# Kernel optimization log

Hardware: AMD Instinct MI355X
Metric: run time of the kernel (lower is better)

## Reference

```python
import jax, jax.numpy as jnp
import numpy as np

B, L, D, H = 2, 2048, 1024, 16
HD = D // H
KW = 4  # conv kernel width


def layernorm(x, g, b, eps=1e-5):
    m = jnp.mean(x, axis=-1, keepdims=True)
    v = jnp.var(x, axis=-1, keepdims=True)
    return (x - m) / jnp.sqrt(v + eps) * g + b


def causal_conv(x, w, b):
    # torch Conv1d(k=4, padding=3, groups=D) then truncate to L => causal depthwise conv
    # out[t] = sum_j w[:, j] * x[t - 3 + j] + b
    xp = jnp.pad(x, ((0, 0), (KW - 1, 0), (0, 0)))
    Lx = x.shape[1]
    out = b
    for j in range(KW):
        out = out + xp[:, j:j + Lx, :] * w[:, j]
    return out


def setup_inputs() -> dict:
    key = jax.random.key(0)
    ks = jax.random.split(key, 16)
    r = lambda i, shape, s=0.02: jax.random.normal(ks[i], shape, jnp.float32) * s
    return dict(
        x=r(0, (B, L, D), 1.0),
        Wqkv=r(1, (D, 3 * D)), Wout=r(2, (D, D)),
        Wgate=r(3, (D, D)), bgate=jnp.zeros((D,), jnp.float32),
        fn_g=jnp.ones((D,), jnp.float32), fn_b=jnp.zeros((D,), jnp.float32),
        dn_g=jnp.ones((D,), jnp.float32), dn_b=jnp.zeros((D,), jnp.float32),
        dWq=r(4, (D, D)), dWk=r(5, (D, D)), dWv=r(6, (D, D)), dWo=r(7, (D, D)),
        Wbeta=r(8, (D, H)), bbeta=jnp.zeros((H,), jnp.float32),
        cq_w=r(9, (D, KW), 0.1), cq_b=jnp.zeros((D,), jnp.float32),
        ck_w=r(10, (D, KW), 0.1), ck_b=jnp.zeros((D,), jnp.float32),
        ln_g=jnp.ones((D,), jnp.float32), ln_b=jnp.zeros((D,), jnp.float32),
    )


def _delta_scan(q, k, v, beta):
    # q,k,v: (B,L,H,HD) ; beta: (B,L,H)
    Bx = q.shape[0]
    S0 = jnp.zeros((Bx, H, HD, HD), q.dtype)
    z0 = jnp.zeros((Bx, H, HD), q.dtype)

    def step(carry, inp):
        S, z = carry
        q_t, k_t, v_t, b_t = inp  # (B,H,HD) x3, (B,H)
        y = jnp.einsum('bhij,bhj->bhi', S, q_t)
        denom = jnp.einsum('bhi,bhi->bh', z, q_t)[..., None] + 1e-6
        y = y / denom
        old = jnp.einsum('bhij,bhj->bhi', S, k_t)
        delta = v_t - old
        S = S + b_t[..., None, None] * jnp.einsum('bhi,bhj->bhij', delta, k_t)
        z = z + b_t[..., None] * k_t
        return (S, z), y

    xs = (jnp.moveaxis(q, 1, 0), jnp.moveaxis(k, 1, 0),
          jnp.moveaxis(v, 1, 0), jnp.moveaxis(beta, 1, 0))
    (S, z), ys = jax.lax.scan(step, (S0, z0), xs)
    return jnp.moveaxis(ys, 0, 1), S, z  # (B,L,H,HD)


def _forward(x, Wqkv, Wout, Wgate, bgate, fn_g, fn_b, dn_g, dn_b,
             dWq, dWk, dWv, dWo, Wbeta, bbeta, cq_w, cq_b, ck_w, ck_b, ln_g, ln_b):
    Bx, Lx, Dx = x.shape
    # ---- flash (full causal, L<=2048 branch) ----
    qkv = (x @ Wqkv).reshape(Bx, Lx, 3, H, HD)
    q = jnp.moveaxis(qkv[:, :, 0], 1, 2)  # (B,H,L,HD)
    k = jnp.moveaxis(qkv[:, :, 1], 1, 2)
    v = jnp.moveaxis(qkv[:, :, 2], 1, 2)
    scale = HD ** -0.5
    scores = jnp.einsum('bhqd,bhkd->bhqk', q, k) * scale
    causal = jnp.tril(jnp.ones((Lx, Lx), bool))
    scores = jnp.where(causal, scores, -jnp.inf)
    attn = jax.nn.softmax(scores, axis=-1)
    flash = jnp.einsum('bhqk,bhkd->bhqd', attn, v)
    flash = jnp.moveaxis(flash, 1, 2).reshape(Bx, Lx, Dx) @ Wout
    flash = layernorm(flash, fn_g, fn_b)
    # ---- delta branch ----
    dq = causal_conv(x @ dWq, cq_w, cq_b).reshape(Bx, Lx, H, HD)
    dk = causal_conv(x @ dWk, ck_w, ck_b).reshape(Bx, Lx, H, HD)
    dv = (x @ dWv).reshape(Bx, Lx, H, HD)
    dk = dk / jnp.maximum(jnp.linalg.norm(dk, axis=-1, keepdims=True), 1e-12)
    beta = jax.nn.sigmoid(x @ Wbeta + bbeta)  # (B,L,H)
    ys, S, z = _delta_scan(dq, dk, dv, beta)
    delta_out = layernorm(ys.reshape(Bx, Lx, Dx) @ dWo, ln_g, ln_b)  # DeltaAttention layer_norm
    delta_out = layernorm(delta_out, dn_g, dn_b)  # hybrid delta_norm
    # ---- gate ----
    gate = jax.nn.sigmoid(x @ Wgate + bgate)
    out = gate * flash + (1.0 - gate) * delta_out
    return out, S, z


def reference(x, Wqkv, Wout, Wgate, bgate, fn_g, fn_b, dn_g, dn_b,
              dWq, dWk, dWv, dWo, Wbeta, bbeta, cq_w, cq_b, ck_w, ck_b, ln_g, ln_b):
    return _forward(x, Wqkv, Wout, Wgate, bgate, fn_g, fn_b, dn_g, dn_b,
                    dWq, dWk, dWv, dWo, Wbeta, bbeta, cq_w, cq_b, ck_w, ck_b, ln_g, ln_b)
```

## Files before the change

kernel.cpp:

```cpp
#include <hip/hip_runtime.h>
#include <hip/hip_bf16.h>

constexpr int B_ = 2, L_ = 2048, D_ = 1024, H_ = 16;

using bf16x8 = __attribute__((ext_vector_type(8))) short;
using f32x4  = __attribute__((ext_vector_type(4))) float;

__device__ __forceinline__ short f2b(float f) {
  union { float f; unsigned int u; } v; v.f = f;
  unsigned int r = (v.u + 0x7FFFu + ((v.u >> 16) & 1u)) >> 16;
  return (short)r;
}
__device__ __forceinline__ float b2f(unsigned short h) {
  union { unsigned int u; float f; } v; v.u = ((unsigned int)h) << 16; return v.f;
}
__device__ __forceinline__ void split2(float x, float y, unsigned int& h, unsigned int& l) {
  unsigned short hx = (unsigned short)f2b(x), hy = (unsigned short)f2b(y);
  h = (unsigned int)hx | ((unsigned int)hy << 16);
  unsigned short lx = (unsigned short)f2b(x - b2f(hx)), ly = (unsigned short)f2b(y - b2f(hy));
  l = (unsigned int)lx | ((unsigned int)ly << 16);
}
__device__ __forceinline__ float dot4(float4 a, float4 b) {
  return a.x * b.x + a.y * b.y + a.z * b.z + a.w * b.w;
}

__global__ __launch_bounds__(256) void tcast(const float* __restrict__ W, short* __restrict__ Wt,
                                             int N, int K) {
  __shared__ float T[64][65];
  int n0 = blockIdx.x * 64, k0 = blockIdx.y * 64;
  int tid = threadIdx.x;
#pragma unroll
  for (int i = 0; i < 16; ++i) {
    int idx = i * 256 + tid;
    int r = idx >> 6, c = idx & 63;
    T[r][c] = W[(size_t)(k0 + r) * N + n0 + c];
  }
  __syncthreads();
#pragma unroll
  for (int i = 0; i < 16; ++i) {
    int idx = i * 256 + tid;
    int rr = idx >> 6, cc = idx & 63;
    Wt[(size_t)(n0 + rr) * K + k0 + cc] = f2b(T[cc][rr]);
  }
}

__global__ __launch_bounds__(256) void tcast2(const float* __restrict__ W1, const float* __restrict__ W2,
                                              short* __restrict__ Wt1, short* __restrict__ Wt2) {
  __shared__ float T[64][65];
  const float* W = blockIdx.z ? W2 : W1;
  short* Wt = blockIdx.z ? Wt2 : Wt1;
  int n0 = blockIdx.x * 64, k0 = blockIdx.y * 64;
  int tid = threadIdx.x;
#pragma unroll
  for (int i = 0; i < 16; ++i) {
    int idx = i * 256 + tid;
    int r = idx >> 6, c = idx & 63;
    T[r][c] = W[(size_t)(k0 + r) * 1024 + n0 + c];
  }
  __syncthreads();
#pragma unroll
  for (int i = 0; i < 16; ++i) {
    int idx = i * 256 + tid;
    int rr = idx >> 6, cc = idx & 63;
    Wt[(size_t)(n0 + rr) * 1024 + k0 + cc] = f2b(T[cc][rr]);
  }
}

__global__ __launch_bounds__(256) void tcast_split2(const float* __restrict__ W1, const float* __restrict__ W2,
                                                    short* __restrict__ Wh1, short* __restrict__ Wl1,
                                                    short* __restrict__ Wh2, short* __restrict__ Wl2) {
  __shared__ float T[64][65];
  const float* W = blockIdx.z ? W2 : W1;
  short* Wh = blockIdx.z ? Wh2 : Wh1;
  short* Wl = blockIdx.z ? Wl2 : Wl1;
  int n0 = blockIdx.x * 64, k0 = blockIdx.y * 64;
  int tid = threadIdx.x;
#pragma unroll
  for (int i = 0; i < 16; ++i) {
    int idx = i * 256 + tid;
    int r = idx >> 6, c = idx & 63;
    T[r][c] = W[(size_t)(k0 + r) * 1024 + n0 + c];
  }
  __syncthreads();
#pragma unroll
  for (int i = 0; i < 16; ++i) {
    int idx = i * 256 + tid;
    int rr = idx >> 6, cc = idx & 63;
    float w = T[cc][rr];
    short h = f2b(w);
    short l = f2b(w - b2f((unsigned short)h));
    size_t o = (size_t)(n0 + rr) * 1024 + k0 + cc;
    Wh[o] = h;
    Wl[o] = l;
  }
}

template <int BN, typename CT>
__device__ __forceinline__ void gemm_bt_body(const float* __restrict__ A, const short* __restrict__ Wt,
                                             CT* __restrict__ C, int N, int K, int bx, int by) {
  constexpr int MT = (BN == 128) ? 4 : 2;
  constexpr int NT = 4;
  __shared__ __align__(16) short As[128 * 32];
  __shared__ __align__(16) short Bs[BN * 32];
  int tid = threadIdx.x;
  int wave = tid >> 6, lane = tid & 63, quad = lane >> 4, l15 = lane & 15;
  int m0 = by * 128, n0 = bx * BN;
  int wm = (BN == 128) ? (wave >> 1) * 64 : wave * 32;
  int wn = (BN == 128) ? (wave & 1) * 64 : 0;
  f32x4 acc[MT][NT];
#pragma unroll
  for (int mt = 0; mt < MT; ++mt)
#pragma unroll
    for (int nt = 0; nt < NT; ++nt) acc[mt][nt] = (f32x4){0.f, 0.f, 0.f, 0.f};

  for (int k0 = 0; k0 < K; k0 += 32) {
    __syncthreads();
#pragma unroll
    for (int i = 0; i < 2; ++i) {
      int chunk = i * 256 + tid;
      int m = chunk >> 2, kc = (chunk & 3) * 8;
      const float* ap = A + (size_t)(m0 + m) * K + k0 + kc;
      float4 a0 = *(const float4*)ap;
      float4 a1 = *(const float4*)(ap + 4);
      __hip_bfloat162 c0 = __float22bfloat162_rn(make_float2(a0.x, a0.y));
      __hip_bfloat162 c1 = __float22bfloat162_rn(make_float2(a0.z, a0.w));
      __hip_bfloat162 c2 = __float22bfloat162_rn(make_float2(a1.x, a1.y));
      __hip_bfloat162 c3 = __float22bfloat162_rn(make_float2(a1.z, a1.w));
      uint4 u;
      u.x = *(unsigned int*)&c0; u.y = *(unsigned int*)&c1;
      u.z = *(unsigned int*)&c2; u.w = *(unsigned int*)&c3;
      *(uint4*)&As[m * 32 + kc] = u;
    }
#pragma unroll
    for (int i = 0; i < BN * 4 / 256; ++i) {
      int chunk = i * 256 + tid;
      int n = chunk >> 2, kc = (chunk & 3) * 8;
      uint4 w = *(const uint4*)(Wt + (size_t)(n0 + n) * K + k0 + kc);
      *(uint4*)&Bs[n * 32 + kc] = w;
    }
    __syncthreads();
    bf16x8 af[MT], bf[NT];
#pragma unroll
    for (int mt = 0; mt < MT; ++mt) af[mt] = *(bf16x8*)&As[(wm + mt * 16 + l15) * 32 + quad * 8];
#pragma unroll
    for (int nt = 0; nt < NT; ++nt) bf[nt] = *(bf16x8*)&Bs[(wn + nt * 16 + l15) * 32 + quad * 8];
#pragma unroll
    for (int mt = 0; mt < MT; ++mt)
#pragma unroll
      for (int nt = 0; nt < NT; ++nt)
        acc[mt][nt] = __builtin_amdgcn_mfma_f32_16x16x32_bf16(af[mt], bf[nt], acc[mt][nt], 0, 0, 0);
  }
#pragma unroll
  for (int mt = 0; mt < MT; ++mt)
#pragma unroll
    for (int nt = 0; nt < NT; ++nt)
#pragma unroll
      for (int r = 0; r < 4; ++r) {
        size_t idx = (size_t)(m0 + wm + mt * 16 + quad * 4 + r) * N + n0 + wn + nt * 16 + l15;
        if constexpr (sizeof(CT) == 2) C[idx] = f2b(acc[mt][nt][r]);
        else C[idx] = acc[mt][nt][r];
      }
}

template <int BN>
__global__ __launch_bounds__(256) void gemm_bt(const float* __restrict__ A, const short* __restrict__ Wt,
                                               float* __restrict__ C, int N, int K) {
  gemm_bt_body<BN, float>(A, Wt, C, N, K, blockIdx.x, blockIdx.y);
}

__global__ __launch_bounds__(256) void gemm_bt_h(const float* __restrict__ A, const short* __restrict__ Wt,
                                                 short* __restrict__ C, int N, int K) {
  gemm_bt_body<128, short>(A, Wt, C, N, K, blockIdx.x, blockIdx.y);
}

__global__ __launch_bounds__(256) void gemm_bt2(const float* __restrict__ A, const short* __restrict__ Wt1,
                                                const short* __restrict__ Wt2, float* __restrict__ C1,
                                                float* __restrict__ C2) {
  gemm_bt_body<64, float>(A, blockIdx.z ? Wt2 : Wt1, blockIdx.z ? C2 : C1, 1024, 1024,
                          blockIdx.x, blockIdx.y);
}

__global__ __launch_bounds__(256) void gemm_bt_split2(const float* __restrict__ A,
                                                      const short* __restrict__ Wh1, const short* __restrict__ Wl1,
                                                      const short* __restrict__ Wh2, const short* __restrict__ Wl2,
                                                      float* __restrict__ C1, float* __restrict__ C2) {
  constexpr int K = 1024, N = 1024;
  const short* Wh = blockIdx.z ? Wh2 : Wh1;
  const short* Wl = blockIdx.z ? Wl2 : Wl1;
  float* C = blockIdx.z ? C2 : C1;
  __shared__ __align__(16) short Ash[128 * 32];
  __shared__ __align__(16) short Asl[128 * 32];
  __shared__ __align__(16) short Bsh[64 * 32];
  __shared__ __align__(16) short Bsl[64 * 32];
  int tid = threadIdx.x;
  int wave = tid >> 6, lane = tid & 63, quad = lane >> 4, l15 = lane & 15;
  int m0 = blockIdx.y * 128, n0 = blockIdx.x * 64;
  int wm = wave * 32;
  f32x4 acc[2][4];
#pragma unroll
  for (int mt = 0; mt < 2; ++mt)
#pragma unroll
    for (int nt = 0; nt < 4; ++nt) acc[mt][nt] = (f32x4){0.f, 0.f, 0.f, 0.f};

  for (int k0 = 0; k0 < K; k0 += 32) {
    __syncthreads();
#pragma unroll
    for (int i = 0; i < 2; ++i) {
      int chunk = i * 256 + tid;
      int m = chunk >> 2, kc = (chunk & 3) * 8;
      const float* ap = A + (size_t)(m0 + m) * K + k0 + kc;
      float4 a0 = *(const float4*)ap;
      float4 a1 = *(const float4*)(ap + 4);
      uint4 uh, ul;
      split2(a0.x, a0.y, uh.x, ul.x);
      split2(a0.z, a0.w, uh.y, ul.y);
      split2(a1.x, a1.y, uh.z, ul.z);
      split2(a1.z, a1.w, uh.w, ul.w);
      *(uint4*)&Ash[m * 32 + kc] = uh;
      *(uint4*)&Asl[m * 32 + kc] = ul;
    }
    {
      int n = tid >> 2, kc = (tid & 3) * 8;
      size_t off = (size_t)(n0 + n) * K + k0 + kc;
      *(uint4*)&Bsh[n * 32 + kc] = *(const uint4*)(Wh + off);
      *(uint4*)&Bsl[n * 32 + kc] = *(const uint4*)(Wl + off);
    }
    __syncthreads();
    bf16x8 ah[2], al[2], bh[4], bl[4];
#pragma unroll
    for (int mt = 0; mt < 2; ++mt) {
      ah[mt] = *(bf16x8*)&Ash[(wm + mt * 16 + l15) * 32 + quad * 8];
      al[mt] = *(bf16x8*)&Asl[(wm + mt * 16 + l15) * 32 + quad * 8];
    }
#pragma unroll
    for (int nt = 0; nt < 4; ++nt) {
      bh[nt] = *(bf16x8*)&Bsh[(nt * 16 + l15) * 32 + quad * 8];
      bl[nt] = *(bf16x8*)&Bsl[(nt * 16 + l15) * 32 + quad * 8];
    }
#pragma unroll
    for (int mt = 0; mt < 2; ++mt)
#pragma unroll
      for (int nt = 0; nt < 4; ++nt) {
        f32x4 a = acc[mt][nt];
        a = __builtin_amdgcn_mfma_f32_16x16x32_bf16(al[mt], bh[nt], a, 0, 0, 0);
        a = __builtin_amdgcn_mfma_f32_16x16x32_bf16(ah[mt], bl[nt], a, 0, 0, 0);
        a = __builtin_amdgcn_mfma_f32_16x16x32_bf16(ah[mt], bh[nt], a, 0, 0, 0);
        acc[mt][nt] = a;
      }
  }
#pragma unroll
  for (int mt = 0; mt < 2; ++mt)
#pragma unroll
    for (int nt = 0; nt < 4; ++nt)
#pragma unroll
      for (int r = 0; r < 4; ++r) {
        size_t idx = (size_t)(m0 + wm + mt * 16 + quad * 4 + r) * N + n0 + nt * 16 + l15;
        C[idx] = acc[mt][nt][r];
      }
}

__global__ __launch_bounds__(256) void attn_mfma(const short* __restrict__ qkv, float* __restrict__ outp) {
  __shared__ __align__(16) short Kl[64 * 64];
  __shared__ __align__(16) short Vt[64 * 64];
  __shared__ __align__(16) short Pl[64 * 64];
  int qb = 31 - blockIdx.x, h = blockIdx.y, b = blockIdx.z;
  int tid = threadIdx.x;
  int wave = tid >> 6, lane = tid & 63;
  int quad = lane >> 4, l15 = lane & 15;
  int qrow = qb * 64 + wave * 16 + l15;
  bf16x8 qf[2];
  {
    const short* qbase = qkv + (size_t)(b * L_ + qrow) * 3072 + h * 64;
#pragma unroll
    for (int s = 0; s < 2; ++s) qf[s] = *(const bf16x8*)(qbase + s * 32 + quad * 8);
  }
  f32x4 Of[4];
  float mrow[4], lrow[4], alpha[4];
#pragma unroll
  for (int dt = 0; dt < 4; ++dt) Of[dt] = (f32x4){0.f, 0.f, 0.f, 0.f};
#pragma unroll
  for (int r = 0; r < 4; ++r) { mrow[r] = -1e30f; lrow[r] = 0.f; }

  for (int kt = 0; kt <= qb; ++kt) {
    __syncthreads();
#pragma unroll
    for (int it = 0; it < 2; ++it) {
      int e8 = tid + it * 256;
      int key = e8 >> 3, g = e8 & 7;
      const short* src = qkv + ((size_t)((b * L_ + kt * 64 + key) * 3) + 1) * 1024 + h * 64 + g * 8;
      *(bf16x8*)&Kl[key * 64 + ((g ^ (key & 7)) << 3)] = *(const bf16x8*)src;
    }
    {
      int key4 = tid >> 4;
      int d4 = tid & 15;
      const short* vsrc = qkv + ((size_t)((b * L_ + kt * 64 + key4 * 4) * 3) + 2) * 1024 + h * 64 + d4 * 4;
      short4 v0 = *(const short4*)vsrc;
      short4 v1 = *(const short4*)(vsrc + 3072);
      short4 v2 = *(const short4*)(vsrc + 6144);
      short4 v3 = *(const short4*)(vsrc + 9216);
      short vr0[4] = {v0.x, v0.y, v0.z, v0.w};
      short vr1[4] = {v1.x, v1.y, v1.z, v1.w};
      short vr2[4] = {v2.x, v2.y, v2.z, v2.w};
      short vr3[4] = {v3.x, v3.y, v3.z, v3.w};
      int kg = key4 >> 1, k7b = (key4 & 1) * 4;
#pragma unroll
      for (int jj = 0; jj < 4; ++jj) {
        int d = d4 * 4 + jj;
        short4 sv;
        sv.x = vr0[jj]; sv.y = vr1[jj]; sv.z = vr2[jj]; sv.w = vr3[jj];
        *(short4*)&Vt[d * 64 + ((kg ^ (d & 7)) << 3) + k7b] = sv;
      }
    }
    __syncthreads();
    f32x4 sc[4];
#pragma unroll
    for (int nt = 0; nt < 4; ++nt) sc[nt] = (f32x4){0.f, 0.f, 0.f, 0.f};
#pragma unroll
    for (int s = 0; s < 2; ++s) {
#pragma unroll
      for (int nt = 0; nt < 4; ++nt) {
        int key = nt * 16 + l15;
        bf16x8 kf = *(bf16x8*)&Kl[key * 64 + (((4 * s + quad) ^ (key & 7)) << 3)];
        sc[nt] = __builtin_amdgcn_mfma_f32_16x16x32_bf16(qf[s], kf, sc[nt], 0, 0, 0);
      }
    }
    bool diag = (kt == qb);
#pragma unroll
    for (int r = 0; r < 4; ++r) {
      float sv[4];
#pragma unroll
      for (int nt = 0; nt < 4; ++nt) {
        float v = sc[nt][r] * 0.125f;
        if (diag && (nt * 16 + l15 > wave * 16 + quad * 4 + r)) v = -1e30f;
        sv[nt] = v;
      }
      float mx = fmaxf(fmaxf(sv[0], sv[1]), fmaxf(sv[2], sv[3]));
      mx = fmaxf(mx, __shfl_xor(mx, 1));
      mx = fmaxf(mx, __shfl_xor(mx, 2));
      mx = fmaxf(mx, __shfl_xor(mx, 4));
      mx = fmaxf(mx, __shfl_xor(mx, 8));
      float mnew = fmaxf(mrow[r], mx);
      float al = __expf(mrow[r] - mnew);
      mrow[r] = mnew;
      alpha[r] = al;
      int prow = wave * 16 + quad * 4 + r;
      int r7 = prow & 7;
      float ps = 0.f;
#pragma unroll
      for (int nt = 0; nt < 4; ++nt) {
        float p = __expf(sv[nt] - mnew);
        ps += p;
        Pl[prow * 64 + ((((nt << 1) + (l15 >> 3)) ^ r7) << 3) + (l15 & 7)] = f2b(p);
      }
      ps += __shfl_xor(ps, 1);
      ps += __shfl_xor(ps, 2);
      ps += __shfl_xor(ps, 4);
      ps += __shfl_xor(ps, 8);
      lrow[r] = lrow[r] * al + ps;
    }
#pragma unroll
    for (int dt = 0; dt < 4; ++dt)
#pragma unroll
      for (int r = 0; r < 4; ++r) Of[dt][r] *= alpha[r];
#pragma unroll
    for (int s = 0; s < 2; ++s) {
      bf16x8 pf = *(bf16x8*)&Pl[(wave * 16 + l15) * 64 + (((4 * s + quad) ^ (l15 & 7)) << 3)];
#pragma unroll
      for (int dt = 0; dt < 4; ++dt) {
        int d = dt * 16 + l15;
        bf16x8 vf = *(bf16x8*)&Vt[d * 64 + (((4 * s + quad) ^ (d & 7)) << 3)];
        Of[dt] = __builtin_amdgcn_mfma_f32_16x16x32_bf16(pf, vf, Of[dt], 0, 0, 0);
      }
    }
  }
#pragma unroll
  for (int r = 0; r < 4; ++r) alpha[r] = 1.f / lrow[r];
  int orow = qb * 64 + wave * 16 + quad * 4;
#pragma unroll
  for (int dt = 0; dt < 4; ++dt)
#pragma unroll
    for (int r = 0; r < 4; ++r)
      outp[(size_t)(b * L_ + orow + r) * 1024 + h * 64 + dt * 16 + l15] = Of[dt][r] * alpha[r];
}

__global__ __launch_bounds__(256) void ln_kernel(float* __restrict__ X, const float* __restrict__ g,
                                                 const float* __restrict__ bb) {
  int row = blockIdx.x, tid = threadIdx.x;
  float* xr = X + (size_t)row * D_;
  float v[4], s = 0.f, ss = 0.f;
#pragma unroll
  for (int i = 0; i < 4; ++i) { v[i] = xr[tid + i * 256]; s += v[i]; ss += v[i] * v[i]; }
#pragma unroll
  for (int off = 32; off; off >>= 1) { s += __shfl_xor(s, off); ss += __shfl_xor(ss, off); }
  __shared__ float rs[4], rss[4];
  if ((tid & 63) == 0) { rs[tid >> 6] = s; rss[tid >> 6] = ss; }
  __syncthreads();
  float S = rs[0] + rs[1] + rs[2] + rs[3];
  float SS = rss[0] + rss[1] + rss[2] + rss[3];
  float mean = S * (1.f / 1024.f);
  float var = SS * (1.f / 1024.f) - mean * mean;
  float inv = rsqrtf(var + 1e-5f);
#pragma unroll
  for (int i = 0; i < 4; ++i) {
    int c = tid + i * 256;
    xr[c] = (v[i] - mean) * inv * g[c] + bb[c];
  }
}

__global__ __launch_bounds__(256) void ln2mix_kernel(const float* __restrict__ X,
                                                     const float* __restrict__ g1, const float* __restrict__ b1,
                                                     const float* __restrict__ g2, const float* __restrict__ b2,
                                                     const float* __restrict__ gpre, const float* __restrict__ bgate,
                                                     const float* __restrict__ fo, float* __restrict__ outp) {
  int row = blockIdx.x, tid = threadIdx.x;
  const float* xr = X + (size_t)row * D_;
  __shared__ float rs[4], rss[4];
  float v[4], s = 0.f, ss = 0.f;
#pragma unroll
  for (int i = 0; i < 4; ++i) { v[i] = xr[tid + i * 256]; s += v[i]; ss += v[i] * v[i]; }
#pragma unroll
  for (int off = 32; off; off >>= 1) { s += __shfl_xor(s, off); ss += __shfl_xor(ss, off); }
  if ((tid & 63) == 0) { rs[tid >> 6] = s; rss[tid >> 6] = ss; }
  __syncthreads();
  float S = rs[0] + rs[1] + rs[2] + rs[3];
  float SS = rss[0] + rss[1] + rss[2] + rss[3];
  float mean = S * (1.f / 1024.f);
  float var = SS * (1.f / 1024.f) - mean * mean;
  float inv = rsqrtf(var + 1e-5f);
  s = 0.f; ss = 0.f;
#pragma unroll
  for (int i = 0; i < 4; ++i) {
    int c = tid + i * 256;
    v[i] = (v[i] - mean) * inv * g1[c] + b1[c];
    s += v[i]; ss += v[i] * v[i];
  }
#pragma unroll
  for (int off = 32; off; off >>= 1) { s += __shfl_xor(s, off); ss += __shfl_xor(ss, off); }
  __syncthreads();
  if ((tid & 63) == 0) { rs[tid >> 6] = s; rss[tid >> 6] = ss; }
  __syncthreads();
  S = rs[0] + rs[1] + rs[2] + rs[3];
  SS = rss[0] + rss[1] + rss[2] + rss[3];
  mean = S * (1.f / 1024.f);
  var = SS * (1.f / 1024.f) - mean * mean;
  inv = rsqrtf(var + 1e-5f);
#pragma unroll
  for (int i = 0; i < 4; ++i) {
    int c = tid + i * 256;
    size_t idx = (size_t)row * D_ + c;
    float w = (v[i] - mean) * inv * g2[c] + b2[c];
    float gg = 1.f / (1.f + __expf(-(gpre[idx] + bgate[c])));
    outp[idx] = gg * fo[idx] + (1.f - gg) * w;
  }
}

__global__ __launch_bounds__(256) void convnorm_kernel(const float* __restrict__ qin, const float* __restrict__ kin,
                                                       const float* __restrict__ qw, const float* __restrict__ qb,
                                                       const float* __restrict__ kw, const float* __restrict__ kb,
                                                       float* __restrict__ qout, float* __restrict__ kout) {
  int path = blockIdx.y;
  int row = blockIdx.x * 4 + (threadIdx.x >> 6);
  int lane = threadIdx.x & 63;
  int bl = row >> 4, h = row & 15;
  int t = bl & (L_ - 1);
  int d = h * 64 + lane;
  size_t idx = (size_t)bl * D_ + d;
  const float* xin = path ? kin : qin;
  const float* w = path ? kw : qw;
  const float* bias = path ? kb : qb;
  float acc = bias[d];
#pragma unroll
  for (int j = 0; j < 4; ++j) {
    int tt = t - 3 + j;
    if (tt >= 0) acc += w[d * 4 + j] * xin[idx + (size_t)(j - 3) * D_];
  }
  if (path) {
    float n2 = acc * acc;
#pragma unroll
    for (int off = 32; off; off >>= 1) n2 += __shfl_xor(n2, off);
    acc = acc / fmaxf(sqrtf(n2), 1e-12f);
    kout[idx] = acc;
  } else {
    qout[idx] = acc;
  }
}

__global__ __launch_bounds__(256) void beta_kernel(const float* __restrict__ xf, const float* __restrict__ Wb,
                                                   const float* __restrict__ bb, float* __restrict__ beta) {
  int row = blockIdx.x, tid = threadIdx.x;
  int h = tid & 15, seg = tid >> 4;
  const float* xr = xf + (size_t)row * D_ + seg * 64;
  const float* wp = Wb + (seg * 64) * H_ + h;
  float p = 0.f;
  for (int k = 0; k < 64; ++k) p += xr[k] * wp[k * H_];
  __shared__ float red[16][17];
  red[seg][h] = p;
  __syncthreads();
  if (tid < 16) {
    float s = bb[tid];
#pragma unroll
    for (int s2 = 0; s2 < 16; ++s2) s += red[s2][tid];
    beta[(size_t)row * H_ + tid] = 1.f / (1.f + __expf(-s));
  }
}

__global__ __launch_bounds__(256) void prep_kernel(const float* __restrict__ dq, const float* __restrict__ dk,
                                                   const float* __restrict__ beta,
                                                   float* __restrict__ Minv_g, float* __restrict__ Bq_g) {
  __shared__ __align__(16) float Kl[32 * 68];
  __shared__ __align__(16) float Ql[32 * 68];
  __shared__ __align__(16) float Ml[32 * 36];
  __shared__ __align__(16) float Xl[32 * 36];
  __shared__ __align__(16) float bl[32];
  int c = blockIdx.x, bh = blockIdx.y;
  int b = bh >> 4, h = bh & 15;
  int t0 = c * 32;
  int tid = threadIdx.x;
#pragma unroll
  for (int rep = 0; rep < 2; ++rep) {
    int id = tid * 2 + rep;
    int r = id >> 4, j4 = id & 15;
    size_t gi = (size_t)(b * L_ + t0 + r) * 1024 + h * 64 + j4 * 4;
    *(float4*)&Kl[r * 68 + j4 * 4] = *(const float4*)&dk[gi];
    *(float4*)&Ql[r * 68 + j4 * 4] = *(const float4*)&dq[gi];
  }
  if (tid < 32) bl[tid] = beta[(size_t)(b * L_ + t0 + tid) * 16 + h];
  __syncthreads();
  int t = tid >> 3, s0 = (tid & 7) * 4;
  float accA[4] = {0.f, 0.f, 0.f, 0.f}, accB[4] = {0.f, 0.f, 0.f, 0.f};
#pragma unroll
  for (int k4 = 0; k4 < 16; ++k4) {
    float4 kt = *(float4*)&Kl[t * 68 + k4 * 4];
    float4 qt = *(float4*)&Ql[t * 68 + k4 * 4];
#pragma unroll
    for (int j = 0; j < 4; ++j) {
      float4 ks = *(float4*)&Kl[(s0 + j) * 68 + k4 * 4];
      accA[j] += dot4(kt, ks);
      accB[j] += dot4(qt, ks);
    }
  }
  float4 bq;
  float* bqp = (float*)&bq;
#pragma unroll
  for (int j = 0; j < 4; ++j) {
    int s = s0 + j;
    Ml[t * 36 + s] = (s < t) ? bl[t] * accA[j] : ((s == t) ? 1.f : 0.f);
    bqp[j] = (s < t) ? accB[j] : 0.f;
  }
  size_t obase = ((size_t)(bh * 64 + c) * 32 + t) * 32 + s0;
  *(float4*)&Bq_g[obase] = bq;
  __syncthreads();
  if (tid < 32) {
    int col = tid;
    float xr[32];
#pragma unroll
    for (int tt = 0; tt < 32; ++tt) {
      float x = (tt == col) ? 1.f : 0.f;
#pragma unroll
      for (int s = 0; s < tt; ++s) x -= Ml[tt * 36 + s] * xr[s];
      xr[tt] = x;
      Xl[tt * 36 + col] = x;
    }
  }
  __syncthreads();
  float4 mv = make_float4(Xl[t * 36 + s0], Xl[t * 36 + s0 + 1], Xl[t * 36 + s0 + 2], Xl[t * 36 + s0 + 3]);
  *(float4*)&Minv_g[obase] = mv;
}

__global__ __launch_bounds__(256) void delta_kernel(const float* __restrict__ dq, const float* __restrict__ dk,
                                                    const float* __restrict__ dv, const float* __restrict__ beta,
                                                    const float* __restrict__ Minv_g, const float* __restrict__ Bq_g,
                                                    float* __restrict__ ys, float* __restrict__ outS,
                                                    float* __restrict__ outZ) {
  __shared__ __align__(16) float Kl[2][32 * 68];
  __shared__ __align__(16) float Ql[2][32 * 68];
  __shared__ __align__(16) float Vl[2][32 * 9];
  __shared__ __align__(16) float Mil[2][32 * 36];
  __shared__ __align__(16) float Bql[2][32 * 36];
  __shared__ __align__(16) float bl[2][32];
  __shared__ __align__(16) float S0l[8 * 68];
  __shared__ __align__(16) float Y0l[32 * 9];
  __shared__ __align__(16) float RtmpTl[8 * 36];
  __shared__ __align__(16) float RTl[8 * 36];
  __shared__ __align__(16) float z0l[68];
  __shared__ __align__(16) float qzl[32];
  __shared__ __align__(16) float denl[32];
  int bh = blockIdx.x & 31, grp = blockIdx.x >> 5;
  int b = bh >> 4, h = bh & 15;
  int i0 = grp * 8;
  int tid = threadIdx.x;
  int r = tid >> 3, j8 = (tid & 7) * 8, s4 = tid & 7;
  size_t kqbase = (size_t)(b * L_) * 1024 + h * 64;

  for (int e = tid; e < 8 * 68; e += 256) S0l[e] = 0.f;
  if (tid < 68) z0l[tid] = 0.f;

  float4 kA, kB, qA, qB, mr, br;
  float vr, blr = 0.f;
  {
    const float* kp = dk + kqbase + (size_t)r * 1024 + j8;
    kA = ((const float4*)kp)[0]; kB = ((const float4*)kp)[1];
    const float* qp = dq + kqbase + (size_t)r * 1024 + j8;
    qA = ((const float4*)qp)[0]; qB = ((const float4*)qp)[1];
    size_t gb = ((size_t)(bh * 64) * 32 + r) * 32 + s4 * 4;
    mr = *(const float4*)&Minv_g[gb];
    br = *(const float4*)&Bq_g[gb];
    vr = dv[(size_t)(b * L_ + r) * 1024 + h * 64 + i0 + s4];
    if (tid < 32) blr = beta[(size_t)(b * L_ + tid) * 16 + h];
  }
  *(float4*)&Kl[0][r * 68 + j8] = kA; *(float4*)&Kl[0][r * 68 + j8 + 4] = kB;
  *(float4*)&Ql[0][r * 68 + j8] = qA; *(float4*)&Ql[0][r * 68 + j8 + 4] = qB;
  *(float4*)&Mil[0][r * 36 + s4 * 4] = mr;
  *(float4*)&Bql[0][r * 36 + s4 * 4] = br;
  Vl[0][r * 9 + s4] = vr;
  if (tid < 32) bl[0][tid] = blr;
  __syncthreads();

  for (int c = 0; c < 64; ++c) {
    int cur = c & 1, nxt = cur ^ 1;
    int cn = (c + 1 < 64) ? c + 1 : 63;
    int t0n = cn * 32;
    {
      const float* kp = dk + kqbase + (size_t)(t0n + r) * 1024 + j8;
      kA = ((const float4*)kp)[0]; kB = ((const float4*)kp)[1];
      const float* qp = dq + kqbase + (size_t)(t0n + r) * 1024 + j8;
      qA = ((const float4*)qp)[0]; qB = ((const float4*)qp)[1];
      size_t gb = ((size_t)(bh * 64 + cn) * 32 + r) * 32 + s4 * 4;
      mr = *(const float4*)&Minv_g[gb];
      br = *(const float4*)&Bq_g[gb];
      vr = dv[(size_t)(b * L_ + t0n + r) * 1024 + h * 64 + i0 + s4];
      if (tid < 32) blr = beta[(size_t)(b * L_ + t0n + tid) * 16 + h];
    }
    int t0 = c * 32;
    {
      int rr = tid >> 3;
      int iq = (tid >> 1) & 3;
      int jh = tid & 1;
      float aK0 = 0.f, aK1 = 0.f, aY0 = 0.f, aY1 = 0.f;
#pragma unroll
      for (int jj = 0; jj < 8; ++jj) {
        int j4 = jh * 8 + jj;
        float4 k = *(float4*)&Kl[cur][rr * 68 + j4 * 4];
        float4 q = *(float4*)&Ql[cur][rr * 68 + j4 * 4];
        float4 sA = *(float4*)&S0l[iq * 68 + j4 * 4];
        float4 sB = *(float4*)&S0l[(iq + 4) * 68 + j4 * 4];
        aK0 += dot4(k, sA); aK1 += dot4(k, sB);
        aY0 += dot4(q, sA); aY1 += dot4(q, sB);
      }
      aK0 += __shfl_xor(aK0, 1); aK1 += __shfl_xor(aK1, 1);
      aY0 += __shfl_xor(aY0, 1); aY1 += __shfl_xor(aY1, 1);
      if (jh == 0) {
        float be = bl[cur][rr];
        RtmpTl[iq * 36 + rr] = be * (Vl[cur][rr * 9 + iq] - aK0);
        RtmpTl[(iq + 4) * 36 + rr] = be * (Vl[cur][rr * 9 + iq + 4] - aK1);
        Y0l[rr * 9 + iq] = aY0;
        Y0l[rr * 9 + iq + 4] = aY1;
      }
      if (tid < 32) {
        float a = 0.f;
#pragma unroll
        for (int j4 = 0; j4 < 16; ++j4) {
          float4 q = *(float4*)&Ql[cur][tid * 68 + j4 * 4];
          float4 z = *(float4*)&z0l[j4 * 4];
          a += dot4(q, z);
        }
        qzl[tid] = a;
      }
    }
    __syncthreads();
    {
      int t = tid >> 3, i = tid & 7;
      float acc = 0.f;
#pragma unroll
      for (int s4i = 0; s4i < 8; ++s4i) {
        float4 m = *(float4*)&Mil[cur][t * 36 + s4i * 4];
        float4 rt = *(float4*)&RtmpTl[i * 36 + s4i * 4];
        acc += dot4(m, rt);
      }
      RTl[i * 36 + t] = acc;
      if (tid < 32) {
        float a = qzl[tid];
#pragma unroll
        for (int s4i = 0; s4i < 8; ++s4i) {
          float4 bq = *(float4*)&Bql[cur][tid * 36 + s4i * 4];
          float4 be = *(float4*)&bl[cur][s4i * 4];
          a += dot4(bq, be);
        }
        denl[tid] = a + 1e-6f;
      }
    }
    __syncthreads();
    {
      int t = tid >> 3, i = tid & 7;
      float acc = 0.f;
#pragma unroll
      for (int s4i = 0; s4i < 8; ++s4i) {
        float4 bq = *(float4*)&Bql[cur][t * 36 + s4i * 4];
        float4 rt = *(float4*)&RTl[i * 36 + s4i * 4];
        acc += dot4(bq, rt);
      }
      float y = (Y0l[t * 9 + i] + acc) / denl[t];
      ys[(size_t)(b * L_ + t0 + t) * 1024 + h * 64 + i0 + i] = y;
    }
    {
      int i = tid >> 5;
      int j2 = (tid & 31) * 2;
      float a0 = S0l[i * 68 + j2];
      float a1 = S0l[i * 68 + j2 + 1];
#pragma unroll
      for (int s4i = 0; s4i < 8; ++s4i) {
        float4 rt = *(float4*)&RTl[i * 36 + s4i * 4];
        float2 k0 = *(float2*)&Kl[cur][(s4i * 4 + 0) * 68 + j2];
        float2 k1 = *(float2*)&Kl[cur][(s4i * 4 + 1) * 68 + j2];
        float2 k2 = *(float2*)&Kl[cur][(s4i * 4 + 2) * 68 + j2];
        float2 k3 = *(float2*)&Kl[cur][(s4i * 4 + 3) * 68 + j2];
        a0 += rt.x * k0.x + rt.y * k1.x + rt.z * k2.x + rt.w * k3.x;
        a1 += rt.x * k0.y + rt.y * k1.y + rt.z * k2.y + rt.w * k3.y;
      }
      S0l[i * 68 + j2] = a0;
      S0l[i * 68 + j2 + 1] = a1;
    }
    if (tid < 64) {
      float a = z0l[tid];
#pragma unroll
      for (int s = 0; s < 32; ++s) a += bl[cur][s] * Kl[cur][s * 68 + tid];
      z0l[tid] = a;
    }
    *(float4*)&Kl[nxt][r * 68 + j8] = kA; *(float4*)&Kl[nxt][r * 68 + j8 + 4] = kB;
    *(float4*)&Ql[nxt][r * 68 + j8] = qA; *(float4*)&Ql[nxt][r * 68 + j8 + 4] = qB;
    *(float4*)&Mil[nxt][r * 36 + s4 * 4] = mr;
    *(float4*)&Bql[nxt][r * 36 + s4 * 4] = br;
    Vl[nxt][r * 9 + s4] = vr;
    if (tid < 32) bl[nxt][tid] = blr;
    __syncthreads();
  }
  {
    int i = tid >> 5, j2 = (tid & 31) * 2;
    *(float2*)&outS[((size_t)(bh * 64) + i0 + i) * 64 + j2] = *(float2*)&S0l[i * 68 + j2];
  }
  if (grp == 0 && tid < 64) outZ[bh * 64 + tid] = z0l[tid];
}

extern "C" void kernel_launch(void* const* d_in, const int* in_sizes, int n_in,
                              void* d_out, int out_size, void* d_ws, size_t ws_size,
                              hipStream_t stream) {
  const float* x     = (const float*)d_in[0];
  const float* Wqkv  = (const float*)d_in[1];
  const float* Wout  = (const float*)d_in[2];
  const float* Wgate = (const float*)d_in[3];
  const float* bgate = (const float*)d_in[4];
  const float* fn_g  = (const float*)d_in[5];
  const float* fn_b  = (const float*)d_in[6];
  const float* dn_g  = (const float*)d_in[7];
  const float* dn_b  = (const float*)d_in[8];
  const float* dWq   = (const float*)d_in[9];
  const float* dWk   = (const float*)d_in[10];
  const float* dWv   = (const float*)d_in[11];
  const float* dWo   = (const float*)d_in[12];
  const float* Wbeta = (const float*)d_in[13];
  const float* bbeta = (const float*)d_in[14];
  const float* cq_w  = (const float*)d_in[15];
  const float* cq_b  = (const float*)d_in[16];
  const float* ck_w  = (const float*)d_in[17];
  const float* ck_b  = (const float*)d_in[18];
  const float* ln_g  = (const float*)d_in[19];
  const float* ln_b  = (const float*)d_in[20];

  float* ws = (float*)d_ws;
  short* qkvh   = (short*)ws;
  float* dv     = ws;
  float* dqc    = ws + 4194304;
  float* dkc    = ws + 8388608;
  float* attnO  = ws + 12582912;
  short* wtg    = (short*)(ws + 12582912);
  short* Wvt    = (short*)(ws + 14680064);
  float* Minv_g = ws + 12582912;
  float* Bq_g   = ws + 14680064;
  float* do1    = ws + 12582912;
  float* fo     = ws + 16777216;
  float* dqp    = ws + 20971520;
  float* gpre   = ws + 20971520;
  float* dkp    = ws + 25165824;
  float* ysb    = ws + 25165824;
  float* betab  = ws + 29360128;

  short* Wqkvt = (short*)(ws + 20971520);
  short* Woutt = (short*)(ws + 29426688);
  short* Wot   = (short*)(ws + 4194304);

  short* Wqh = (short*)(ws + 8388608);
  short* Wql = (short*)(ws + 8912896);
  short* Wkh = (short*)(ws + 9437184);
  short* Wkl = (short*)(ws + 9961472);

  float* out  = (float*)d_out;
  float* outS = out + 4194304;
  float* outZ = out + 4325376;

  tcast<<<dim3(48, 16), 256, 0, stream>>>(Wqkv, Wqkvt, 3072, 1024);
  gemm_bt_h<<<dim3(24, 32), 256, 0, stream>>>(x, Wqkvt, qkvh, 3072, 1024);
  attn_mfma<<<dim3(32, H_, B_), 256, 0, stream>>>(qkvh, attnO);
  tcast<<<dim3(16, 16), 256, 0, stream>>>(Wout, Woutt, 1024, 1024);
  gemm_bt<64><<<dim3(16, 32), 256, 0, stream>>>(attnO, Woutt, fo, 1024, 1024);
  ln_kernel<<<4096, 256, 0, stream>>>(fo, fn_g, fn_b);
  tcast_split2<<<dim3(16, 16, 2), 256, 0, stream>>>(dWq, dWk, Wqh, Wql, Wkh, Wkl);
  gemm_bt_split2<<<dim3(16, 32, 2), 256, 0, stream>>>(x, Wqh, Wql, Wkh, Wkl, dqp, dkp);
  convnorm_kernel<<<dim3(16384, 2), 256, 0, stream>>>(dqp, dkp, cq_w, cq_b, ck_w, ck_b, dqc, dkc);
  beta_kernel<<<4096, 256, 0, stream>>>(x, Wbeta, bbeta, betab);
  tcast2<<<dim3(16, 16, 2), 256, 0, stream>>>(dWv, Wgate, Wvt, wtg);
  gemm_bt2<<<dim3(16, 32, 2), 256, 0, stream>>>(x, Wvt, wtg, dv, gpre);
  prep_kernel<<<dim3(64, 32), 256, 0, stream>>>(dqc, dkc, betab, Minv_g, Bq_g);
  delta_kernel<<<256, 256, 0, stream>>>(dqc, dkc, dv, betab, Minv_g, Bq_g, ysb, outS, outZ);
  tcast<<<dim3(16, 16), 256, 0, stream>>>(dWo, Wot, 1024, 1024);
  gemm_bt<64><<<dim3(16, 32), 256, 0, stream>>>(ysb, Wot, do1, 1024, 1024);
  ln2mix_kernel<<<4096, 256, 0, stream>>>(do1, ln_g, ln_b, dn_g, dn_b, gpre, bgate, fo, out);
}
```

Measured before the change: 806.3 us.

## Split delta scan over more blocks with 4 state rows each, single-buffer LDS

The delta-rule chunked scan kernel now assigns 4 rows of the state matrix per block instead of 8, doubling the grid from 256 to 512 blocks to fill more compute units on the sequential chunk loop. Shared-memory double buffering is dropped in favor of single buffers plus an extra barrier before staging the next chunk, shrinking LDS use. Each block still redundantly loads the full K, Q, Minv and Bq tiles and recomputes the z/denominator, so global traffic for those grows, and half the threads sit idle in several phases.

Result: faster. 778.2 us (-3.5%).

```diff
diff --git a/kernel.cpp b/kernel.cpp
--- a/kernel.cpp
+++ b/kernel.cpp
@@ -572,31 +572,31 @@
                                                     const float* __restrict__ Minv_g, const float* __restrict__ Bq_g,
                                                     float* __restrict__ ys, float* __restrict__ outS,
                                                     float* __restrict__ outZ) {
-  __shared__ __align__(16) float Kl[2][32 * 68];
-  __shared__ __align__(16) float Ql[2][32 * 68];
-  __shared__ __align__(16) float Vl[2][32 * 9];
-  __shared__ __align__(16) float Mil[2][32 * 36];
-  __shared__ __align__(16) float Bql[2][32 * 36];
-  __shared__ __align__(16) float bl[2][32];
-  __shared__ __align__(16) float S0l[8 * 68];
-  __shared__ __align__(16) float Y0l[32 * 9];
-  __shared__ __align__(16) float RtmpTl[8 * 36];
-  __shared__ __align__(16) float RTl[8 * 36];
+  __shared__ __align__(16) float Kl[32 * 68];
+  __shared__ __align__(16) float Ql[32 * 68];
+  __shared__ __align__(16) float Vl[32 * 5];
+  __shared__ __align__(16) float Mil[32 * 36];
+  __shared__ __align__(16) float Bql[32 * 36];
+  __shared__ __align__(16) float bl[32];
+  __shared__ __align__(16) float S0l[4 * 68];
+  __shared__ __align__(16) float Y0l[32 * 5];
+  __shared__ __align__(16) float RtmpTl[4 * 36];
+  __shared__ __align__(16) float RTl[4 * 36];
   __shared__ __align__(16) float z0l[68];
   __shared__ __align__(16) float qzl[32];
   __shared__ __align__(16) float denl[32];
   int bh = blockIdx.x & 31, grp = blockIdx.x >> 5;
   int b = bh >> 4, h = bh & 15;
-  int i0 = grp * 8;
+  int i0 = grp * 4;
   int tid = threadIdx.x;
   int r = tid >> 3, j8 = (tid & 7) * 8, s4 = tid & 7;
   size_t kqbase = (size_t)(b * L_) * 1024 + h * 64;
 
-  for (int e = tid; e < 8 * 68; e += 256) S0l[e] = 0.f;
+  for (int e = tid; e < 4 * 68; e += 256) S0l[e] = 0.f;
   if (tid < 68) z0l[tid] = 0.f;
 
   float4 kA, kB, qA, qB, mr, br;
-  float vr, blr = 0.f;
+  float vr = 0.f, blr = 0.f;
   {
     const float* kp = dk + kqbase + (size_t)r * 1024 + j8;
     kA = ((const float4*)kp)[0]; kB = ((const float4*)kp)[1];
@@ -605,19 +605,18 @@
     size_t gb = ((size_t)(bh * 64) * 32 + r) * 32 + s4 * 4;
     mr = *(const float4*)&Minv_g[gb];
     br = *(const float4*)&Bq_g[gb];
-    vr = dv[(size_t)(b * L_ + r) * 1024 + h * 64 + i0 + s4];
+    if (tid < 128) vr = dv[(size_t)(b * L_ + (tid >> 2)) * 1024 + h * 64 + i0 + (tid & 3)];
     if (tid < 32) blr = beta[(size_t)(b * L_ + tid) * 16 + h];
   }
-  *(float4*)&Kl[0][r * 68 + j8] = kA; *(float4*)&Kl[0][r * 68 + j8 + 4] = kB;
-  *(float4*)&Ql[0][r * 68 + j8] = qA; *(float4*)&Ql[0][r * 68 + j8 + 4] = qB;
-  *(float4*)&Mil[0][r * 36 + s4 * 4] = mr;
-  *(float4*)&Bql[0][r * 36 + s4 * 4] = br;
-  Vl[0][r * 9 + s4] = vr;
-  if (tid < 32) bl[0][tid] = blr;
+  *(float4*)&Kl[r * 68 + j8] = kA; *(float4*)&Kl[r * 68 + j8 + 4] = kB;
+  *(float4*)&Ql[r * 68 + j8] = qA; *(float4*)&Ql[r * 68 + j8 + 4] = qB;
+  *(float4*)&Mil[r * 36 + s4 * 4] = mr;
+  *(float4*)&Bql[r * 36 + s4 * 4] = br;
+  if (tid < 128) Vl[(tid >> 2) * 5 + (tid & 3)] = vr;
+  if (tid < 32) bl[tid] = blr;
   __syncthreads();
 
   for (int c = 0; c < 64; ++c) {
-    int cur = c & 1, nxt = cur ^ 1;
     int cn = (c + 1 < 64) ? c + 1 : 63;
     int t0n = cn * 32;
     {
@@ -628,39 +627,36 @@
       size_t gb = ((size_t)(bh * 64 + cn) * 32 + r) * 32 + s4 * 4;
       mr = *(const float4*)&Minv_g[gb];
       br = *(const float4*)&Bq_g[gb];
-      vr = dv[(size_t)(b * L_ + t0n + r) * 1024 + h * 64 + i0 + s4];
+      if (tid < 128) vr = dv[(size_t)(b * L_ + t0n + (tid >> 2)) * 1024 + h * 64 + i0 + (tid & 3)];
       if (tid < 32) blr = beta[(size_t)(b * L_ + t0n + tid) * 16 + h];
     }
     int t0 = c * 32;
     {
-      int rr = tid >> 3;
-      int iq = (tid >> 1) & 3;
       int jh = tid & 1;
-      float aK0 = 0.f, aK1 = 0.f, aY0 = 0.f, aY1 = 0.f;
+      int i = (tid >> 1) & 3;
+      int t = tid >> 3;
+      float aK = 0.f, aY = 0.f;
 #pragma unroll
       for (int jj = 0; jj < 8; ++jj) {
         int j4 = jh * 8 + jj;
-        float4 k = *(float4*)&Kl[cur][rr * 68 + j4 * 4];
-        float4 q = *(float4*)&Ql[cur][rr * 68 + j4 * 4];
-        float4 sA = *(float4*)&S0l[iq * 68 + j4 * 4];
-        float4 sB = *(float4*)&S0l[(iq + 4) * 68 + j4 * 4];
-        aK0 += dot4(k, sA); aK1 += dot4(k, sB);
-        aY0 += dot4(q, sA); aY1 += dot4(q, sB);
-      }
-      aK0 += __shfl_xor(aK0, 1); aK1 += __shfl_xor(aK1, 1);
-      aY0 += __shfl_xor(aY0, 1); aY1 += __shfl_xor(aY1, 1);
+        float4 k = *(float4*)&Kl[t * 68 + j4 * 4];
+        float4 q = *(float4*)&Ql[t * 68 + j4 * 4];
+        float4 s = *(float4*)&S0l[i * 68 + j4 * 4];
+        aK += dot4(k, s);
+        aY += dot4(q, s);
+      }
+      aK += __shfl_xor(aK, 1);
+      aY += __shfl_xor(aY, 1);
       if (jh == 0) {
-        float be = bl[cur][rr];
-        RtmpTl[iq * 36 + rr] = be * (Vl[cur][rr * 9 + iq] - aK0);
-        RtmpTl[(iq + 4) * 36 + rr] = be * (Vl[cur][rr * 9 + iq + 4] - aK1);
-        Y0l[rr * 9 + iq] = aY0;
-        Y0l[rr * 9 + iq + 4] = aY1;
+        float be = bl[t];
+        RtmpTl[i * 36 + t] = be * (Vl[t * 5 + i] - aK);
+        Y0l[t * 5 + i] = aY;
       }
       if (tid < 32) {
         float a = 0.f;
 #pragma unroll
         for (int j4 = 0; j4 < 16; ++j4) {
-          float4 q = *(float4*)&Ql[cur][tid * 68 + j4 * 4];
+          float4 q = *(float4*)&Ql[tid * 68 + j4 * 4];
           float4 z = *(float4*)&z0l[j4 * 4];
           a += dot4(q, z);
         }
@@ -669,74 +665,73 @@
     }
     __syncthreads();
     {
-      int t = tid >> 3, i = tid & 7;
-      float acc = 0.f;
-#pragma unroll
-      for (int s4i = 0; s4i < 8; ++s4i) {
-        float4 m = *(float4*)&Mil[cur][t * 36 + s4i * 4];
-        float4 rt = *(float4*)&RtmpTl[i * 36 + s4i * 4];
-        acc += dot4(m, rt);
-      }
-      RTl[i * 36 + t] = acc;
-      if (tid < 32) {
-        float a = qzl[tid];
+      if (tid < 128) {
+        int t = tid >> 2, i = tid & 3;
+        float acc = 0.f;
 #pragma unroll
         for (int s4i = 0; s4i < 8; ++s4i) {
-          float4 bq = *(float4*)&Bql[cur][tid * 36 + s4i * 4];
-          float4 be = *(float4*)&bl[cur][s4i * 4];
+          float4 m = *(float4*)&Mil[t * 36 + s4i * 4];
+          float4 rt = *(float4*)&RtmpTl[i * 36 + s4i * 4];
+          acc += dot4(m, rt);
+        }
+        RTl[i * 36 + t] = acc;
+      } else if (tid < 160) {
+        int t = tid - 128;
+        float a = qzl[t];
+#pragma unroll
+        for (int s4i = 0; s4i < 8; ++s4i) {
+          float4 bq = *(float4*)&Bql[t * 36 + s4i * 4];
+          float4 be = *(float4*)&bl[s4i * 4];
           a += dot4(bq, be);
         }
-        denl[tid] = a + 1e-6f;
-      }
-    }
-    __syncthreads();
-    {
-      int t = tid >> 3, i = tid & 7;
+        denl[t] = a + 1e-6f;
+      }
+    }
+    __syncthreads();
+    if (tid < 128) {
+      int t = tid >> 2, i = tid & 3;
       float acc = 0.f;
 #pragma unroll
       for (int s4i = 0; s4i < 8; ++s4i) {
-        float4 bq = *(float4*)&Bql[cur][t * 36 + s4i * 4];
+        float4 bq = *(float4*)&Bql[t * 36 + s4i * 4];
         float4 rt = *(float4*)&RTl[i * 36 + s4i * 4];
         acc += dot4(bq, rt);
       }
-      float y = (Y0l[t * 9 + i] + acc) / denl[t];
+      float y = (Y0l[t * 5 + i] + acc) / denl[t];
       ys[(size_t)(b * L_ + t0 + t) * 1024 + h * 64 + i0 + i] = y;
     }
     {
-      int i = tid >> 5;
-      int j2 = (tid & 31) * 2;
-      float a0 = S0l[i * 68 + j2];
-      float a1 = S0l[i * 68 + j2 + 1];
+      int i = tid >> 6, j = tid & 63;
+      float a = S0l[i * 68 + j];
 #pragma unroll
       for (int s4i = 0; s4i < 8; ++s4i) {
         float4 rt = *(float4*)&RTl[i * 36 + s4i * 4];
-        float2 k0 = *(float2*)&Kl[cur][(s4i * 4 + 0) * 68 + j2];
-        float2 k1 = *(float2*)&Kl[cur][(s4i * 4 + 1) * 68 + j2];
-        float2 k2 = *(float2*)&Kl[cur][(s4i * 4 + 2) * 68 + j2];
-        float2 k3 = *(float2*)&Kl[cur][(s4i * 4 + 3) * 68 + j2];
-        a0 += rt.x * k0.x + rt.y * k1.x + rt.z * k2.x + rt.w * k3.x;
-        a1 += rt.x * k0.y + rt.y * k1.y + rt.z * k2.y + rt.w * k3.y;
-      }
-      S0l[i * 68 + j2] = a0;
-      S0l[i * 68 + j2 + 1] = a1;
-    }
-    if (tid < 64) {
-      float a = z0l[tid];
-#pragma unroll
-      for (int s = 0; s < 32; ++s) a += bl[cur][s] * Kl[cur][s * 68 + tid];
-      z0l[tid] = a;
-    }
-    *(float4*)&Kl[nxt][r * 68 + j8] = kA; *(float4*)&Kl[nxt][r * 68 + j8 + 4] = kB;
-    *(float4*)&Ql[nxt][r * 68 + j8] = qA; *(float4*)&Ql[nxt][r * 68 + j8 + 4] = qB;
-    *(float4*)&Mil[nxt][r * 36 + s4 * 4] = mr;
-    *(float4*)&Bql[nxt][r * 36 + s4 * 4] = br;
-    Vl[nxt][r * 9 + s4] = vr;
-    if (tid < 32) bl[nxt][tid] = blr;
+        a += rt.x * Kl[(s4i * 4 + 0) * 68 + j]
+           + rt.y * Kl[(s4i * 4 + 1) * 68 + j]
+           + rt.z * Kl[(s4i * 4 + 2) * 68 + j]
+           + rt.w * Kl[(s4i * 4 + 3) * 68 + j];
+      }
+      S0l[i * 68 + j] = a;
+    }
+    if (tid >= 128 && tid < 192) {
+      int j = tid - 128;
+      float a = z0l[j];
+#pragma unroll
+      for (int s = 0; s < 32; ++s) a += bl[s] * Kl[s * 68 + j];
+      z0l[j] = a;
+    }
+    __syncthreads();
+    *(float4*)&Kl[r * 68 + j8] = kA; *(float4*)&Kl[r * 68 + j8 + 4] = kB;
+    *(float4*)&Ql[r * 68 + j8] = qA; *(float4*)&Ql[r * 68 + j8 + 4] = qB;
+    *(float4*)&Mil[r * 36 + s4 * 4] = mr;
+    *(float4*)&Bql[r * 36 + s4 * 4] = br;
+    if (tid < 128) Vl[(tid >> 2) * 5 + (tid & 3)] = vr;
+    if (tid < 32) bl[tid] = blr;
     __syncthreads();
   }
   {
-    int i = tid >> 5, j2 = (tid & 31) * 2;
-    *(float2*)&outS[((size_t)(bh * 64) + i0 + i) * 64 + j2] = *(float2*)&S0l[i * 68 + j2];
+    int i = tid >> 6, j = tid & 63;
+    outS[((size_t)(bh * 64) + i0 + i) * 64 + j] = S0l[i * 68 + j];
   }
   if (grp == 0 && tid < 64) outZ[bh * 64 + tid] = z0l[tid];
 }
@@ -810,7 +805,7 @@
   tcast2<<<dim3(16, 16, 2), 256, 0, stream>>>(dWv, Wgate, Wvt, wtg);
   gemm_bt2<<<dim3(16, 32, 2), 256, 0, stream>>>(x, Wvt, wtg, dv, gpre);
   prep_kernel<<<dim3(64, 32), 256, 0, stream>>>(dqc, dkc, betab, Minv_g, Bq_g);
-  delta_kernel<<<256, 256, 0, stream>>>(dqc, dkc, dv, betab, Minv_g, Bq_g, ysb, outS, outZ);
+  delta_kernel<<<512, 256, 0, stream>>>(dqc, dkc, dv, betab, Minv_g, Bq_g, ysb, outS, outZ);
   tcast<<<dim3(16, 16), 256, 0, stream>>>(dWo, Wot, 1024, 1024);
   gemm_bt<64><<<dim3(16, 32), 256, 0, stream>>>(ysb, Wot, do1, 1024, 1024);
   ln2mix_kernel<<<4096, 256, 0, stream>>>(do1, ln_g, ln_b, dn_g, dn_b, gpre, bgate, fo, out);
```
